# Kernel optimization log

Hardware: AMD Instinct MI355X
Metric: run time of the kernel (lower is better)

Reference implementation:

```python
import jax, jax.numpy as jnp
from jax import lax
import numpy as np

INPUT_SIZE = 1
HIDDEN = 32
NUM_LAYERS = 2
OUTPUT_SIZE = 1
FC1 = 16
B, T = 4096, 512


def _lstm_layer(x, w_ih, w_hh, b_ih, b_hh):
    """One LSTM layer, batch_first x: [B,T,in] -> outputs [B,T,H], (h_T, c_T).
    PyTorch gate order: i, f, g, o."""
    Bsz = x.shape[0]
    H = w_hh.shape[1]
    # Precompute input projections for all timesteps: [B,T,4H]
    xp = jnp.einsum('bti,gi->btg', x, w_ih) + b_ih + b_hh
    xp_t = jnp.swapaxes(xp, 0, 1)  # [T,B,4H]

    def step(carry, xt):
        h, c = carry
        gates = xt + h @ w_hh.T  # [B,4H]
        i, f, g, o = jnp.split(gates, 4, axis=-1)
        i = jax.nn.sigmoid(i)
        f = jax.nn.sigmoid(f)
        g = jnp.tanh(g)
        o = jax.nn.sigmoid(o)
        c = f * c + i * g
        h = o * jnp.tanh(c)
        return (h, c), h

    h0 = jnp.zeros((Bsz, H), dtype=x.dtype)
    c0 = jnp.zeros((Bsz, H), dtype=x.dtype)
    (hT, cT), hs = lax.scan(step, (h0, c0), xp_t)
    return jnp.swapaxes(hs, 0, 1), (hT, cT)


def setup_inputs() -> dict:
    key = jax.random.key(0)
    ks = jax.random.split(key, 12)
    s = 1.0 / np.sqrt(HIDDEN)

    def u(k, shape):
        return jax.random.uniform(k, shape, jnp.float32, -s, s)

    x = jax.random.normal(ks[0], (B, T, INPUT_SIZE), jnp.float32)
    return {
        'x': x,
        'w_ih0': u(ks[1], (4 * HIDDEN, INPUT_SIZE)),
        'w_hh0': u(ks[2], (4 * HIDDEN, HIDDEN)),
        'b_ih0': u(ks[3], (4 * HIDDEN,)),
        'b_hh0': u(ks[4], (4 * HIDDEN,)),
        'w_ih1': u(ks[5], (4 * HIDDEN, HIDDEN)),
        'w_hh1': u(ks[6], (4 * HIDDEN, HIDDEN)),
        'b_ih1': u(ks[7], (4 * HIDDEN,)),
        'b_hh1': u(ks[8], (4 * HIDDEN,)),
        'fc1_w': u(ks[9], (FC1, HIDDEN)),
        'fc1_b': jnp.zeros((FC1,), jnp.float32),
        'fc2_w': u(ks[10], (OUTPUT_SIZE, FC1)),
        'fc2_b': jnp.zeros((OUTPUT_SIZE,), jnp.float32),
    }


def reference(x, w_ih0, w_hh0, b_ih0, b_hh0, w_ih1, w_hh1, b_ih1, b_hh1,
              fc1_w, fc1_b, fc2_w, fc2_b):
    # Layer 0: need full output sequence to feed layer 1.
    h_seq, _ = _lstm_layer(x, w_ih0, w_hh0, b_ih0, b_hh0)
    # (inter-layer dropout is identity at inference)
    # Layer 1: only final hidden state is used downstream.
    _, (hT, _) = _lstm_layer(h_seq, w_ih1, w_hh1, b_ih1, b_hh1)
    # Head (dropouts identity at inference): fc1 -> relu -> fc2
    out = jax.nn.relu(hT @ fc1_w.T + fc1_b)
    out = out @ fc2_w.T + fc2_b  # [B, output_size]
    return out
```

## Files before the change

### kernel.cpp

```cpp
#include <hip/hip_runtime.h>

#define TLEN 512
#define XSTR 516
#define HSTR 40

typedef __attribute__((ext_vector_type(8))) short bf16x8;
typedef __attribute__((ext_vector_type(4))) float f32x4;

#define LOG2E_ 1.44269504f
#define S2F_   2.88539008f

__device__ __forceinline__ float fexp2_(float x) {
#if __has_builtin(__builtin_amdgcn_exp2f)
    return __builtin_amdgcn_exp2f(x);
#else
    return __expf(x * 0.69314718056f);
#endif
}
__device__ __forceinline__ float frcp_(float x) {
#if __has_builtin(__builtin_amdgcn_rcpf)
    return __builtin_amdgcn_rcpf(x);
#else
    return 1.0f / x;
#endif
}
__device__ __forceinline__ unsigned short f2bf(float f) {
    unsigned u = __float_as_uint(f);
    u += 0x7FFFu + ((u >> 16) & 1u);
    return (unsigned short)(u >> 16);
}
__device__ __forceinline__ float bf2f(unsigned short b) {
    return __uint_as_float(((unsigned)b) << 16);
}

__device__ __forceinline__ float lstm_nl(const f32x4 a, float& cS) {
    const float i_ = frcp_(1.0f + fexp2_(a[0]));
    const float f_ = frcp_(1.0f + fexp2_(a[1]));
    const float rg = frcp_(1.0f + fexp2_(a[2]));
    const float g_ = S2F_ - 2.0f * S2F_ * rg;
    const float o_ = frcp_(1.0f + fexp2_(a[3]));
    cS = f_ * cS + i_ * g_;
    const float rc = frcp_(1.0f + fexp2_(cS));
    return o_ * (1.0f - 2.0f * rc);
}

__global__ __launch_bounds__(512, 1)
void lstm2_mfma(const float* __restrict__ x,
                const float* __restrict__ w_ih0,
                const float* __restrict__ w_hh0,
                const float* __restrict__ b_ih0,
                const float* __restrict__ b_hh0,
                const float* __restrict__ w_ih1,
                const float* __restrict__ w_hh1,
                const float* __restrict__ b_ih1,
                const float* __restrict__ b_hh1,
                const float* __restrict__ fc1_w,
                const float* __restrict__ fc1_b,
                const float* __restrict__ fc2_w,
                const float* __restrict__ fc2_b,
                float* __restrict__ out)
{
    __shared__ float x_lds[16][XSTR];
    __shared__ unsigned short h0b[2][2][16][HSTR];
    __shared__ unsigned short h1b[2][2][16][HSTR];
    __shared__ float h1f[16][36];

    const int tid  = threadIdx.x;
    const int wid  = tid >> 6;
    const int lane = tid & 63;
    const int col  = lane & 15;
    const int kq   = lane >> 4;
    const int b0   = blockIdx.x * 16;

    for (int i4 = tid; i4 < (16 * TLEN) / 4; i4 += 512) {
        const int idx = i4 * 4;
        const int row = idx >> 9, cx = idx & 511;
        float4 v = *(const float4*)(x + (long)(b0 + row) * TLEN + cx);
        *(float4*)&x_lds[row][cx] = v;
    }
    for (int i = tid; i < 2 * 2 * 16 * HSTR; i += 512) {
        ((unsigned short*)h0b)[i] = 0;
        ((unsigned short*)h1b)[i] = 0;
    }

    const int tile = wid;
    const int jj   = 4 * tile + kq;
    const int k0   = kq * 8;

    const int   arow = (col & 3) * 32 + 4 * tile + (col >> 2);
    const float sA   = ((col & 3) == 2) ? S2F_ : -LOG2E_;

    bf16x8 wL0hi, wL0lo, wIhi, wIlo, wHhi, wHlo;
    #pragma unroll
    for (int e = 0; e < 8; ++e) {
        float w;
        unsigned short hb;
        w = sA * w_hh0[arow * 32 + k0 + e]; hb = f2bf(w);
        wL0hi[e] = (short)hb; wL0lo[e] = (short)f2bf(w - bf2f(hb));
        w = sA * w_ih1[arow * 32 + k0 + e]; hb = f2bf(w);
        wIhi[e]  = (short)hb; wIlo[e]  = (short)f2bf(w - bf2f(hb));
        w = sA * w_hh1[arow * 32 + k0 + e]; hb = f2bf(w);
        wHhi[e]  = (short)hb; wHlo[e]  = (short)f2bf(w - bf2f(hb));
    }

    f32x4 biasL0, biasL1, xwv;
    #pragma unroll
    for (int r = 0; r < 4; ++r) {
        const int  row = r * 32 + 4 * tile + kq;
        const float sr = (r == 2) ? S2F_ : -LOG2E_;
        biasL0[r] = sr * (b_ih0[row] + b_hh0[row]);
        biasL1[r] = sr * (b_ih1[row] + b_hh1[row]);
        xwv[r]    = sr * w_ih0[row];
    }

    float cL0 = 0.0f, cL1 = 0.0f;
    __syncthreads();

#define PACK_H(BUF, PAR, HV, J)                                                  \
    do {                                                                         \
        const unsigned u_ = __float_as_uint(HV);                                 \
        BUF[PAR][0][col][J] = (unsigned short)(u_ >> 16);                        \
        const float lof_ = (HV) - __uint_as_float(u_ & 0xFFFF0000u);             \
        BUF[PAR][1][col][J] = (unsigned short)(__float_as_uint(lof_) >> 16);     \
    } while (0)

#define STEP_BODY(T, CUR, PRV)                                                   \
    do {                                                                         \
        const int t_ = (T);                                                      \
        const bf16x8 bhi = *(const bf16x8*)&h0b[PRV][0][col][k0];                \
        const bf16x8 blo = *(const bf16x8*)&h0b[PRV][1][col][k0];                \
        if (t_ < TLEN) {                                                         \
            const float xt = x_lds[col][t_];                                     \
            f32x4 aL0 = biasL0 + xwv * xt;                                       \
            aL0 = __builtin_amdgcn_mfma_f32_16x16x32_bf16(wL0hi, bhi, aL0, 0, 0, 0); \
            aL0 = __builtin_amdgcn_mfma_f32_16x16x32_bf16(wL0hi, blo, aL0, 0, 0, 0); \
            aL0 = __builtin_amdgcn_mfma_f32_16x16x32_bf16(wL0lo, bhi, aL0, 0, 0, 0); \
            const float hv = lstm_nl(aL0, cL0);                                  \
            PACK_H(h0b, CUR, hv, jj);                                            \
        }                                                                        \
        if (t_ >= 1) {                                                           \
            const bf16x8 chi = *(const bf16x8*)&h1b[CUR][0][col][k0];            \
            const bf16x8 clo = *(const bf16x8*)&h1b[CUR][1][col][k0];            \
            f32x4 aL1 = biasL1;                                                  \
            aL1 = __builtin_amdgcn_mfma_f32_16x16x32_bf16(wIhi, bhi, aL1, 0, 0, 0); \
            aL1 = __builtin_amdgcn_mfma_f32_16x16x32_bf16(wIhi, blo, aL1, 0, 0, 0); \
            aL1 = __builtin_amdgcn_mfma_f32_16x16x32_bf16(wIlo, bhi, aL1, 0, 0, 0); \
            aL1 = __builtin_amdgcn_mfma_f32_16x16x32_bf16(wHhi, chi, aL1, 0, 0, 0); \
            aL1 = __builtin_amdgcn_mfma_f32_16x16x32_bf16(wHhi, clo, aL1, 0, 0, 0); \
            aL1 = __builtin_amdgcn_mfma_f32_16x16x32_bf16(wHlo, chi, aL1, 0, 0, 0); \
            const float hv = lstm_nl(aL1, cL1);                                  \
            PACK_H(h1b, PRV, hv, jj);                                            \
            if (t_ == TLEN) h1f[col][jj] = hv;                                   \
        }                                                                        \
        __syncthreads();                                                         \
    } while (0)

    STEP_BODY(0, 0, 1);
    for (int tt = 1; tt < TLEN; tt += 2) {
        STEP_BODY(tt,     1, 0);
        STEP_BODY(tt + 1, 0, 1);
    }
#undef STEP_BODY
#undef PACK_H

    if (wid == 0) {
        float s = 0.0f;
        #pragma unroll
        for (int it = 0; it < 4; ++it) {
            const int r = kq * 4 + it;
            float acc = fc1_b[r];
            #pragma unroll
            for (int qq = 0; qq < 8; ++qq) {
                const float4 wv = *(const float4*)(fc1_w + r * 32 + qq * 4);
                const float4 hv = *(const float4*)&h1f[col][qq * 4];
                acc += wv.x * hv.x + wv.y * hv.y + wv.z * hv.z + wv.w * hv.w;
            }
            s += fmaxf(acc, 0.0f) * fc2_w[r];
        }
        s += __shfl_xor(s, 16);
        s += __shfl_xor(s, 32);
        if (lane < 16) out[b0 + col] = s + fc2_b[0];
    }
}

extern "C" void kernel_launch(void* const* d_in, const int* in_sizes, int n_in,
                              void* d_out, int out_size, void* d_ws, size_t ws_size,
                              hipStream_t stream) {
    const float* x     = (const float*)d_in[0];
    const float* w_ih0 = (const float*)d_in[1];
    const float* w_hh0 = (const float*)d_in[2];
    const float* b_ih0 = (const float*)d_in[3];
    const float* b_hh0 = (const float*)d_in[4];
    const float* w_ih1 = (const float*)d_in[5];
    const float* w_hh1 = (const float*)d_in[6];
    const float* b_ih1 = (const float*)d_in[7];
    const float* b_hh1 = (const float*)d_in[8];
    const float* fc1_w = (const float*)d_in[9];
    const float* fc1_b = (const float*)d_in[10];
    const float* fc2_w = (const float*)d_in[11];
    const float* fc2_b = (const float*)d_in[12];
    float* out = (float*)d_out;

    dim3 grid(4096 / 16);
    dim3 block(512);
    hipLaunchKernelGGL(lstm2_mfma, grid, block, 0, stream,
                       x, w_ih0, w_hh0, b_ih0, b_hh0,
                       w_ih1, w_hh1, b_ih1, b_hh1,
                       fc1_w, fc1_b, fc2_w, fc2_b, out);
}
```

Measured before the change: 235.5 us.

## Split LSTM layers across separate wavefronts with 1024-thread blocks

Doubles the block to 16 waves: waves 0-7 compute layer 0 and waves 8-15 compute layer 1, where before each wave did both layers serially in every step. The layer-1 waves split their MFMA chain into two independent accumulators (input and recurrent) and sum them, shortening the dependency chain. The aim is a shorter per-step critical path, at the cost of twice as many waves taking part in each __syncthreads barrier and possibly more register pressure per CU.

```diff
diff --git a/kernel.cpp b/kernel.cpp
--- a/kernel.cpp
+++ b/kernel.cpp
@@ -44,7 +44,7 @@
     return o_ * (1.0f - 2.0f * rc);
 }
 
-__global__ __launch_bounds__(512, 1)
+__global__ __launch_bounds__(1024, 1)
 void lstm2_mfma(const float* __restrict__ x,
                 const float* __restrict__ w_ih0,
                 const float* __restrict__ w_hh0,
@@ -72,48 +72,50 @@
     const int kq   = lane >> 4;
     const int b0   = blockIdx.x * 16;
 
-    for (int i4 = tid; i4 < (16 * TLEN) / 4; i4 += 512) {
+    for (int i4 = tid; i4 < (16 * TLEN) / 4; i4 += 1024) {
         const int idx = i4 * 4;
         const int row = idx >> 9, cx = idx & 511;
         float4 v = *(const float4*)(x + (long)(b0 + row) * TLEN + cx);
         *(float4*)&x_lds[row][cx] = v;
     }
-    for (int i = tid; i < 2 * 2 * 16 * HSTR; i += 512) {
+    for (int i = tid; i < 2 * 2 * 16 * HSTR; i += 1024) {
         ((unsigned short*)h0b)[i] = 0;
         ((unsigned short*)h1b)[i] = 0;
     }
 
-    const int tile = wid;
-    const int jj   = 4 * tile + kq;
-    const int k0   = kq * 8;
+    const bool L0w  = (wid < 8);
+    const int  tile = wid & 7;
+    const int  jj   = 4 * tile + kq;
+    const int  k0   = kq * 8;
 
     const int   arow = (col & 3) * 32 + 4 * tile + (col >> 2);
     const float sA   = ((col & 3) == 2) ? S2F_ : -LOG2E_;
 
-    bf16x8 wL0hi, wL0lo, wIhi, wIlo, wHhi, wHlo;
-    #pragma unroll
-    for (int e = 0; e < 8; ++e) {
-        float w;
-        unsigned short hb;
-        w = sA * w_hh0[arow * 32 + k0 + e]; hb = f2bf(w);
-        wL0hi[e] = (short)hb; wL0lo[e] = (short)f2bf(w - bf2f(hb));
-        w = sA * w_ih1[arow * 32 + k0 + e]; hb = f2bf(w);
-        wIhi[e]  = (short)hb; wIlo[e]  = (short)f2bf(w - bf2f(hb));
-        w = sA * w_hh1[arow * 32 + k0 + e]; hb = f2bf(w);
-        wHhi[e]  = (short)hb; wHlo[e]  = (short)f2bf(w - bf2f(hb));
-    }
-
-    f32x4 biasL0, biasL1, xwv;
+    bf16x8 wAhi, wAlo, wHhi, wHlo;
+    {
+        const float* WA = L0w ? w_hh0 : w_ih1;
+        #pragma unroll
+        for (int e = 0; e < 8; ++e) {
+            float w;
+            unsigned short hb;
+            w = sA * WA[arow * 32 + k0 + e]; hb = f2bf(w);
+            wAhi[e] = (short)hb; wAlo[e] = (short)f2bf(w - bf2f(hb));
+            w = L0w ? 0.0f : sA * w_hh1[arow * 32 + k0 + e]; hb = f2bf(w);
+            wHhi[e] = (short)hb; wHlo[e] = (short)f2bf(w - bf2f(hb));
+        }
+    }
+
+    f32x4 biasv, xwv;
     #pragma unroll
     for (int r = 0; r < 4; ++r) {
         const int  row = r * 32 + 4 * tile + kq;
         const float sr = (r == 2) ? S2F_ : -LOG2E_;
-        biasL0[r] = sr * (b_ih0[row] + b_hh0[row]);
-        biasL1[r] = sr * (b_ih1[row] + b_hh1[row]);
-        xwv[r]    = sr * w_ih0[row];
-    }
-
-    float cL0 = 0.0f, cL1 = 0.0f;
+        biasv[r] = L0w ? sr * (b_ih0[row] + b_hh0[row])
+                       : sr * (b_ih1[row] + b_hh1[row]);
+        xwv[r]   = L0w ? sr * w_ih0[row] : 0.0f;
+    }
+
+    float cS = 0.0f;
     __syncthreads();
 
 #define PACK_H(BUF, PAR, HV, J)                                                  \
@@ -127,30 +129,37 @@
 #define STEP_BODY(T, CUR, PRV)                                                   \
     do {                                                                         \
         const int t_ = (T);                                                      \
-        const bf16x8 bhi = *(const bf16x8*)&h0b[PRV][0][col][k0];                \
-        const bf16x8 blo = *(const bf16x8*)&h0b[PRV][1][col][k0];                \
-        if (t_ < TLEN) {                                                         \
-            const float xt = x_lds[col][t_];                                     \
-            f32x4 aL0 = biasL0 + xwv * xt;                                       \
-            aL0 = __builtin_amdgcn_mfma_f32_16x16x32_bf16(wL0hi, bhi, aL0, 0, 0, 0); \
-            aL0 = __builtin_amdgcn_mfma_f32_16x16x32_bf16(wL0hi, blo, aL0, 0, 0, 0); \
-            aL0 = __builtin_amdgcn_mfma_f32_16x16x32_bf16(wL0lo, bhi, aL0, 0, 0, 0); \
-            const float hv = lstm_nl(aL0, cL0);                                  \
-            PACK_H(h0b, CUR, hv, jj);                                            \
-        }                                                                        \
-        if (t_ >= 1) {                                                           \
-            const bf16x8 chi = *(const bf16x8*)&h1b[CUR][0][col][k0];            \
-            const bf16x8 clo = *(const bf16x8*)&h1b[CUR][1][col][k0];            \
-            f32x4 aL1 = biasL1;                                                  \
-            aL1 = __builtin_amdgcn_mfma_f32_16x16x32_bf16(wIhi, bhi, aL1, 0, 0, 0); \
-            aL1 = __builtin_amdgcn_mfma_f32_16x16x32_bf16(wIhi, blo, aL1, 0, 0, 0); \
-            aL1 = __builtin_amdgcn_mfma_f32_16x16x32_bf16(wIlo, bhi, aL1, 0, 0, 0); \
-            aL1 = __builtin_amdgcn_mfma_f32_16x16x32_bf16(wHhi, chi, aL1, 0, 0, 0); \
-            aL1 = __builtin_amdgcn_mfma_f32_16x16x32_bf16(wHhi, clo, aL1, 0, 0, 0); \
-            aL1 = __builtin_amdgcn_mfma_f32_16x16x32_bf16(wHlo, chi, aL1, 0, 0, 0); \
-            const float hv = lstm_nl(aL1, cL1);                                  \
-            PACK_H(h1b, PRV, hv, jj);                                            \
-            if (t_ == TLEN) h1f[col][jj] = hv;                                   \
+        if (L0w) {                                                               \
+            if (t_ < TLEN) {                                                     \
+                const bf16x8 bhi = *(const bf16x8*)&h0b[PRV][0][col][k0];        \
+                const bf16x8 blo = *(const bf16x8*)&h0b[PRV][1][col][k0];        \
+                const float xt = x_lds[col][t_];                                 \
+                f32x4 a = biasv + xwv * xt;                                      \
+                a = __builtin_amdgcn_mfma_f32_16x16x32_bf16(wAhi, bhi, a, 0, 0, 0); \
+                a = __builtin_amdgcn_mfma_f32_16x16x32_bf16(wAhi, blo, a, 0, 0, 0); \
+                a = __builtin_amdgcn_mfma_f32_16x16x32_bf16(wAlo, bhi, a, 0, 0, 0); \
+                const float hv = lstm_nl(a, cS);                                 \
+                PACK_H(h0b, CUR, hv, jj);                                        \
+            }                                                                    \
+        } else {                                                                 \
+            if (t_ >= 1) {                                                       \
+                const bf16x8 bhi = *(const bf16x8*)&h0b[PRV][0][col][k0];        \
+                const bf16x8 blo = *(const bf16x8*)&h0b[PRV][1][col][k0];        \
+                const bf16x8 chi = *(const bf16x8*)&h1b[CUR][0][col][k0];        \
+                const bf16x8 clo = *(const bf16x8*)&h1b[CUR][1][col][k0];        \
+                f32x4 aI = biasv;                                                \
+                f32x4 aH = {0.0f, 0.0f, 0.0f, 0.0f};                             \
+                aI = __builtin_amdgcn_mfma_f32_16x16x32_bf16(wAhi, bhi, aI, 0, 0, 0); \
+                aH = __builtin_amdgcn_mfma_f32_16x16x32_bf16(wHhi, chi, aH, 0, 0, 0); \
+                aI = __builtin_amdgcn_mfma_f32_16x16x32_bf16(wAhi, blo, aI, 0, 0, 0); \
+                aH = __builtin_amdgcn_mfma_f32_16x16x32_bf16(wHhi, clo, aH, 0, 0, 0); \
+                aI = __builtin_amdgcn_mfma_f32_16x16x32_bf16(wAlo, bhi, aI, 0, 0, 0); \
+                aH = __builtin_amdgcn_mfma_f32_16x16x32_bf16(wHlo, chi, aH, 0, 0, 0); \
+                const f32x4 a = aI + aH;                                         \
+                const float hv = lstm_nl(a, cS);                                 \
+                PACK_H(h1b, PRV, hv, jj);                                        \
+                if (t_ == TLEN) h1f[col][jj] = hv;                               \
+            }                                                                    \
         }                                                                        \
         __syncthreads();                                                         \
     } while (0)
@@ -202,7 +211,7 @@
     float* out = (float*)d_out;
 
     dim3 grid(4096 / 16);
-    dim3 block(512);
+    dim3 block(1024);
     hipLaunchKernelGGL(lstm2_mfma, grid, block, 0, stream,
                        x, w_ih0, w_hh0, b_ih0, b_hh0,
                        w_ih1, w_hh1, b_ih1, b_hh1,
```

Result: slower. 264.4 us (+12.3%).

## Peel LSTM prologue/epilogue and interleave three independent MFMA accumulation chains

Applied to the files above, without the earlier changes.

Peels the first and last timesteps out of the wavefront loop so the steady-state body has no branches. The layer-1 gate sum is split into two independent accumulators (input and recurrent part), and the MFMAs of layer 0, layer-1 input and layer-1 recurrent are interleaved so their dependency chains overlap instead of running as one serial chain of six. The nonlinearities for both layers are computed together to expose more instruction-level parallelism in the exp/rcp sequence. It costs one extra vector add per step and more live registers.

```diff
diff --git a/kernel.cpp b/kernel.cpp
--- a/kernel.cpp
+++ b/kernel.cpp
@@ -33,15 +33,25 @@
     return __uint_as_float(((unsigned)b) << 16);
 }
 
-__device__ __forceinline__ float lstm_nl(const f32x4 a, float& cS) {
-    const float i_ = frcp_(1.0f + fexp2_(a[0]));
-    const float f_ = frcp_(1.0f + fexp2_(a[1]));
-    const float rg = frcp_(1.0f + fexp2_(a[2]));
-    const float g_ = S2F_ - 2.0f * S2F_ * rg;
-    const float o_ = frcp_(1.0f + fexp2_(a[3]));
-    cS = f_ * cS + i_ * g_;
-    const float rc = frcp_(1.0f + fexp2_(cS));
-    return o_ * (1.0f - 2.0f * rc);
+__device__ __forceinline__ void lstm_nl2(const f32x4 a0, const f32x4 a1,
+                                         float& c0, float& c1,
+                                         float& hv0, float& hv1) {
+    const float e00 = fexp2_(a0[0]), e01 = fexp2_(a0[1]);
+    const float e02 = fexp2_(a0[2]), e03 = fexp2_(a0[3]);
+    const float e10 = fexp2_(a1[0]), e11 = fexp2_(a1[1]);
+    const float e12 = fexp2_(a1[2]), e13 = fexp2_(a1[3]);
+    const float i0 = frcp_(1.0f + e00), f0 = frcp_(1.0f + e01);
+    const float r0 = frcp_(1.0f + e02), o0 = frcp_(1.0f + e03);
+    const float i1 = frcp_(1.0f + e10), f1 = frcp_(1.0f + e11);
+    const float r1 = frcp_(1.0f + e12), o1 = frcp_(1.0f + e13);
+    const float g0 = S2F_ - 2.0f * S2F_ * r0;
+    const float g1 = S2F_ - 2.0f * S2F_ * r1;
+    c0 = f0 * c0 + i0 * g0;
+    c1 = f1 * c1 + i1 * g1;
+    const float ec0 = fexp2_(c0), ec1 = fexp2_(c1);
+    const float rc0 = frcp_(1.0f + ec0), rc1 = frcp_(1.0f + ec1);
+    hv0 = o0 * (1.0f - 2.0f * rc0);
+    hv1 = o1 * (1.0f - 2.0f * rc1);
 }
 
 __global__ __launch_bounds__(512, 1)
@@ -124,43 +134,86 @@
         BUF[PAR][1][col][J] = (unsigned short)(__float_as_uint(lof_) >> 16);     \
     } while (0)
 
+    {
+        const bf16x8 bhi = *(const bf16x8*)&h0b[1][0][col][k0];
+        const bf16x8 blo = *(const bf16x8*)&h0b[1][1][col][k0];
+        const float xt = x_lds[col][0];
+        f32x4 aL0 = biasL0 + xwv * xt;
+        aL0 = __builtin_amdgcn_mfma_f32_16x16x32_bf16(wL0hi, bhi, aL0, 0, 0, 0);
+        aL0 = __builtin_amdgcn_mfma_f32_16x16x32_bf16(wL0hi, blo, aL0, 0, 0, 0);
+        aL0 = __builtin_amdgcn_mfma_f32_16x16x32_bf16(wL0lo, bhi, aL0, 0, 0, 0);
+        const float e0 = fexp2_(aL0[0]), e1 = fexp2_(aL0[1]);
+        const float e2 = fexp2_(aL0[2]), e3 = fexp2_(aL0[3]);
+        const float i_ = frcp_(1.0f + e0), f_ = frcp_(1.0f + e1);
+        const float r_ = frcp_(1.0f + e2), o_ = frcp_(1.0f + e3);
+        const float g_ = S2F_ - 2.0f * S2F_ * r_;
+        cL0 = f_ * cL0 + i_ * g_;
+        const float ec = fexp2_(cL0);
+        const float hv = o_ * (1.0f - 2.0f * frcp_(1.0f + ec));
+        PACK_H(h0b, 0, hv, jj);
+        __syncthreads();
+    }
+
 #define STEP_BODY(T, CUR, PRV)                                                   \
     do {                                                                         \
         const int t_ = (T);                                                      \
         const bf16x8 bhi = *(const bf16x8*)&h0b[PRV][0][col][k0];                \
         const bf16x8 blo = *(const bf16x8*)&h0b[PRV][1][col][k0];                \
-        if (t_ < TLEN) {                                                         \
-            const float xt = x_lds[col][t_];                                     \
-            f32x4 aL0 = biasL0 + xwv * xt;                                       \
-            aL0 = __builtin_amdgcn_mfma_f32_16x16x32_bf16(wL0hi, bhi, aL0, 0, 0, 0); \
-            aL0 = __builtin_amdgcn_mfma_f32_16x16x32_bf16(wL0hi, blo, aL0, 0, 0, 0); \
-            aL0 = __builtin_amdgcn_mfma_f32_16x16x32_bf16(wL0lo, bhi, aL0, 0, 0, 0); \
-            const float hv = lstm_nl(aL0, cL0);                                  \
-            PACK_H(h0b, CUR, hv, jj);                                            \
-        }                                                                        \
-        if (t_ >= 1) {                                                           \
-            const bf16x8 chi = *(const bf16x8*)&h1b[CUR][0][col][k0];            \
-            const bf16x8 clo = *(const bf16x8*)&h1b[CUR][1][col][k0];            \
-            f32x4 aL1 = biasL1;                                                  \
-            aL1 = __builtin_amdgcn_mfma_f32_16x16x32_bf16(wIhi, bhi, aL1, 0, 0, 0); \
-            aL1 = __builtin_amdgcn_mfma_f32_16x16x32_bf16(wIhi, blo, aL1, 0, 0, 0); \
-            aL1 = __builtin_amdgcn_mfma_f32_16x16x32_bf16(wIlo, bhi, aL1, 0, 0, 0); \
-            aL1 = __builtin_amdgcn_mfma_f32_16x16x32_bf16(wHhi, chi, aL1, 0, 0, 0); \
-            aL1 = __builtin_amdgcn_mfma_f32_16x16x32_bf16(wHhi, clo, aL1, 0, 0, 0); \
-            aL1 = __builtin_amdgcn_mfma_f32_16x16x32_bf16(wHlo, chi, aL1, 0, 0, 0); \
-            const float hv = lstm_nl(aL1, cL1);                                  \
-            PACK_H(h1b, PRV, hv, jj);                                            \
-            if (t_ == TLEN) h1f[col][jj] = hv;                                   \
-        }                                                                        \
+        const bf16x8 chi = *(const bf16x8*)&h1b[CUR][0][col][k0];                \
+        const bf16x8 clo = *(const bf16x8*)&h1b[CUR][1][col][k0];                \
+        const float xt = x_lds[col][t_];                                         \
+        f32x4 aL0 = biasL0 + xwv * xt;                                           \
+        f32x4 aI  = biasL1;                                                      \
+        f32x4 aH  = {0.0f, 0.0f, 0.0f, 0.0f};                                    \
+        aL0 = __builtin_amdgcn_mfma_f32_16x16x32_bf16(wL0hi, bhi, aL0, 0, 0, 0); \
+        aI  = __builtin_amdgcn_mfma_f32_16x16x32_bf16(wIhi,  bhi, aI,  0, 0, 0); \
+        aH  = __builtin_amdgcn_mfma_f32_16x16x32_bf16(wHhi,  chi, aH,  0, 0, 0); \
+        aL0 = __builtin_amdgcn_mfma_f32_16x16x32_bf16(wL0hi, blo, aL0, 0, 0, 0); \
+        aI  = __builtin_amdgcn_mfma_f32_16x16x32_bf16(wIhi,  blo, aI,  0, 0, 0); \
+        aH  = __builtin_amdgcn_mfma_f32_16x16x32_bf16(wHhi,  clo, aH,  0, 0, 0); \
+        aL0 = __builtin_amdgcn_mfma_f32_16x16x32_bf16(wL0lo, bhi, aL0, 0, 0, 0); \
+        aI  = __builtin_amdgcn_mfma_f32_16x16x32_bf16(wIlo,  bhi, aI,  0, 0, 0); \
+        aH  = __builtin_amdgcn_mfma_f32_16x16x32_bf16(wHlo,  chi, aH,  0, 0, 0); \
+        const f32x4 aL1 = aI + aH;                                               \
+        float hv0, hv1;                                                          \
+        lstm_nl2(aL0, aL1, cL0, cL1, hv0, hv1);                                  \
+        PACK_H(h0b, CUR, hv0, jj);                                               \
+        PACK_H(h1b, PRV, hv1, jj);                                               \
         __syncthreads();                                                         \
     } while (0)
 
-    STEP_BODY(0, 0, 1);
-    for (int tt = 1; tt < TLEN; tt += 2) {
+    for (int tt = 1; tt < TLEN - 1; tt += 2) {
         STEP_BODY(tt,     1, 0);
         STEP_BODY(tt + 1, 0, 1);
     }
+    STEP_BODY(TLEN - 1, 1, 0);
 #undef STEP_BODY
+
+    {
+        const bf16x8 bhi = *(const bf16x8*)&h0b[1][0][col][k0];
+        const bf16x8 blo = *(const bf16x8*)&h0b[1][1][col][k0];
+        const bf16x8 chi = *(const bf16x8*)&h1b[0][0][col][k0];
+        const bf16x8 clo = *(const bf16x8*)&h1b[0][1][col][k0];
+        f32x4 aI = biasL1;
+        f32x4 aH = {0.0f, 0.0f, 0.0f, 0.0f};
+        aI = __builtin_amdgcn_mfma_f32_16x16x32_bf16(wIhi, bhi, aI, 0, 0, 0);
+        aH = __builtin_amdgcn_mfma_f32_16x16x32_bf16(wHhi, chi, aH, 0, 0, 0);
+        aI = __builtin_amdgcn_mfma_f32_16x16x32_bf16(wIhi, blo, aI, 0, 0, 0);
+        aH = __builtin_amdgcn_mfma_f32_16x16x32_bf16(wHhi, clo, aH, 0, 0, 0);
+        aI = __builtin_amdgcn_mfma_f32_16x16x32_bf16(wIlo, bhi, aI, 0, 0, 0);
+        aH = __builtin_amdgcn_mfma_f32_16x16x32_bf16(wHlo, chi, aH, 0, 0, 0);
+        const f32x4 a = aI + aH;
+        const float e0 = fexp2_(a[0]), e1 = fexp2_(a[1]);
+        const float e2 = fexp2_(a[2]), e3 = fexp2_(a[3]);
+        const float i_ = frcp_(1.0f + e0), f_ = frcp_(1.0f + e1);
+        const float r_ = frcp_(1.0f + e2), o_ = frcp_(1.0f + e3);
+        const float g_ = S2F_ - 2.0f * S2F_ * r_;
+        cL1 = f_ * cL1 + i_ * g_;
+        const float ec = fexp2_(cL1);
+        const float hv = o_ * (1.0f - 2.0f * frcp_(1.0f + ec));
+        h1f[col][jj] = hv;
+        __syncthreads();
+    }
 #undef PACK_H
 
     if (wid == 0) {
```

After: 259.4 us. 10.2% more time.

## Split MFMA dependency chains and peel first/last LSTM steps from loop

Applied to the files above, without the earlier changes.

Peels the t=0 and t=TLEN steps out of the recurrent loop so the steady-state body has no branches. The serial MFMA accumulation chains are split into independent accumulators (two for layer 0, three for layer 1) that are summed afterwards, and the layer-0 and layer-1 MFMAs are interleaved. The x value for the next step is prefetched one step early. This shortens the critical MFMA latency chain per timestep, at the cost of extra registers and a slightly different floating-point summation order.

```diff
diff --git a/kernel.cpp b/kernel.cpp
--- a/kernel.cpp
+++ b/kernel.cpp
@@ -34,14 +34,16 @@
 }
 
 __device__ __forceinline__ float lstm_nl(const f32x4 a, float& cS) {
-    const float i_ = frcp_(1.0f + fexp2_(a[0]));
-    const float f_ = frcp_(1.0f + fexp2_(a[1]));
-    const float rg = frcp_(1.0f + fexp2_(a[2]));
-    const float g_ = S2F_ - 2.0f * S2F_ * rg;
-    const float o_ = frcp_(1.0f + fexp2_(a[3]));
+    const float e0 = fexp2_(a[0]), e1 = fexp2_(a[1]);
+    const float e2 = fexp2_(a[2]), e3 = fexp2_(a[3]);
+    const float i_ = frcp_(1.0f + e0);
+    const float f_ = frcp_(1.0f + e1);
+    const float r_ = frcp_(1.0f + e2);
+    const float o_ = frcp_(1.0f + e3);
+    const float g_ = S2F_ - 2.0f * S2F_ * r_;
     cS = f_ * cS + i_ * g_;
-    const float rc = frcp_(1.0f + fexp2_(cS));
-    return o_ * (1.0f - 2.0f * rc);
+    const float ec = fexp2_(cS);
+    return o_ * (1.0f - 2.0f * frcp_(1.0f + ec));
 }
 
 __global__ __launch_bounds__(512, 1)
@@ -112,6 +114,7 @@
         biasL1[r] = sr * (b_ih1[row] + b_hh1[row]);
         xwv[r]    = sr * w_ih0[row];
     }
+    const f32x4 zero4 = {0.0f, 0.0f, 0.0f, 0.0f};
 
     float cL0 = 0.0f, cL1 = 0.0f;
     __syncthreads();
@@ -124,43 +127,71 @@
         BUF[PAR][1][col][J] = (unsigned short)(__float_as_uint(lof_) >> 16);     \
     } while (0)
 
+    float xcur;
+    {
+        const float xt = x_lds[col][0];
+        f32x4 aL0 = biasL0 + xwv * xt;
+        const float hv = lstm_nl(aL0, cL0);
+        PACK_H(h0b, 0, hv, jj);
+        xcur = x_lds[col][1];
+        __syncthreads();
+    }
+
 #define STEP_BODY(T, CUR, PRV)                                                   \
     do {                                                                         \
         const int t_ = (T);                                                      \
         const bf16x8 bhi = *(const bf16x8*)&h0b[PRV][0][col][k0];                \
         const bf16x8 blo = *(const bf16x8*)&h0b[PRV][1][col][k0];                \
-        if (t_ < TLEN) {                                                         \
-            const float xt = x_lds[col][t_];                                     \
-            f32x4 aL0 = biasL0 + xwv * xt;                                       \
-            aL0 = __builtin_amdgcn_mfma_f32_16x16x32_bf16(wL0hi, bhi, aL0, 0, 0, 0); \
-            aL0 = __builtin_amdgcn_mfma_f32_16x16x32_bf16(wL0hi, blo, aL0, 0, 0, 0); \
-            aL0 = __builtin_amdgcn_mfma_f32_16x16x32_bf16(wL0lo, bhi, aL0, 0, 0, 0); \
-            const float hv = lstm_nl(aL0, cL0);                                  \
-            PACK_H(h0b, CUR, hv, jj);                                            \
-        }                                                                        \
-        if (t_ >= 1) {                                                           \
-            const bf16x8 chi = *(const bf16x8*)&h1b[CUR][0][col][k0];            \
-            const bf16x8 clo = *(const bf16x8*)&h1b[CUR][1][col][k0];            \
-            f32x4 aL1 = biasL1;                                                  \
-            aL1 = __builtin_amdgcn_mfma_f32_16x16x32_bf16(wIhi, bhi, aL1, 0, 0, 0); \
-            aL1 = __builtin_amdgcn_mfma_f32_16x16x32_bf16(wIhi, blo, aL1, 0, 0, 0); \
-            aL1 = __builtin_amdgcn_mfma_f32_16x16x32_bf16(wIlo, bhi, aL1, 0, 0, 0); \
-            aL1 = __builtin_amdgcn_mfma_f32_16x16x32_bf16(wHhi, chi, aL1, 0, 0, 0); \
-            aL1 = __builtin_amdgcn_mfma_f32_16x16x32_bf16(wHhi, clo, aL1, 0, 0, 0); \
-            aL1 = __builtin_amdgcn_mfma_f32_16x16x32_bf16(wHlo, chi, aL1, 0, 0, 0); \
-            const float hv = lstm_nl(aL1, cL1);                                  \
-            PACK_H(h1b, PRV, hv, jj);                                            \
-            if (t_ == TLEN) h1f[col][jj] = hv;                                   \
-        }                                                                        \
+        const bf16x8 chi = *(const bf16x8*)&h1b[CUR][0][col][k0];                \
+        const bf16x8 clo = *(const bf16x8*)&h1b[CUR][1][col][k0];                \
+        const float xnext = x_lds[col][t_ + 1];                                  \
+                       \
+        f32x4 a = __builtin_amdgcn_mfma_f32_16x16x32_bf16(wL0hi, bhi, biasL0, 0, 0, 0); \
+        f32x4 bpt = __builtin_amdgcn_mfma_f32_16x16x32_bf16(wL0hi, blo, zero4, 0, 0, 0); \
+        a = __builtin_amdgcn_mfma_f32_16x16x32_bf16(wL0lo, bhi, a, 0, 0, 0);     \
+                                            \
+        f32x4 cch = __builtin_amdgcn_mfma_f32_16x16x32_bf16(wIhi, bhi, biasL1, 0, 0, 0); \
+        f32x4 dch = __builtin_amdgcn_mfma_f32_16x16x32_bf16(wHhi, chi, zero4, 0, 0, 0); \
+        f32x4 ech = __builtin_amdgcn_mfma_f32_16x16x32_bf16(wIhi, blo, zero4, 0, 0, 0); \
+        cch = __builtin_amdgcn_mfma_f32_16x16x32_bf16(wIlo, bhi, cch, 0, 0, 0);  \
+        dch = __builtin_amdgcn_mfma_f32_16x16x32_bf16(wHlo, chi, dch, 0, 0, 0);  \
+        ech = __builtin_amdgcn_mfma_f32_16x16x32_bf16(wHhi, clo, ech, 0, 0, 0);  \
+                      \
+        f32x4 aL0 = a + bpt;                                                     \
+        aL0 += xwv * xcur;                                                       \
+        const float hv0 = lstm_nl(aL0, cL0);                                     \
+        PACK_H(h0b, CUR, hv0, jj);                                               \
+                                                    \
+        const f32x4 aL1 = (cch + dch) + ech;                                     \
+        const float hv1 = lstm_nl(aL1, cL1);                                     \
+        PACK_H(h1b, PRV, hv1, jj);                                               \
+        xcur = xnext;                                                            \
         __syncthreads();                                                         \
     } while (0)
 
-    STEP_BODY(0, 0, 1);
-    for (int tt = 1; tt < TLEN; tt += 2) {
+    for (int tt = 1; tt < TLEN - 1; tt += 2) {
         STEP_BODY(tt,     1, 0);
         STEP_BODY(tt + 1, 0, 1);
     }
+    STEP_BODY(TLEN - 1, 1, 0);
 #undef STEP_BODY
+
+    {
+        const bf16x8 bhi = *(const bf16x8*)&h0b[1][0][col][k0];
+        const bf16x8 blo = *(const bf16x8*)&h0b[1][1][col][k0];
+        const bf16x8 chi = *(const bf16x8*)&h1b[0][0][col][k0];
+        const bf16x8 clo = *(const bf16x8*)&h1b[0][1][col][k0];
+        f32x4 cch = __builtin_amdgcn_mfma_f32_16x16x32_bf16(wIhi, bhi, biasL1, 0, 0, 0);
+        f32x4 dch = __builtin_amdgcn_mfma_f32_16x16x32_bf16(wHhi, chi, zero4, 0, 0, 0);
+        f32x4 ech = __builtin_amdgcn_mfma_f32_16x16x32_bf16(wIhi, blo, zero4, 0, 0, 0);
+        cch = __builtin_amdgcn_mfma_f32_16x16x32_bf16(wIlo, bhi, cch, 0, 0, 0);
+        dch = __builtin_amdgcn_mfma_f32_16x16x32_bf16(wHlo, chi, dch, 0, 0, 0);
+        ech = __builtin_amdgcn_mfma_f32_16x16x32_bf16(wHhi, clo, ech, 0, 0, 0);
+        const f32x4 aL1 = (cch + dch) + ech;
+        const float hv = lstm_nl(aL1, cL1);
+        h1f[col][jj] = hv;
+        __syncthreads();
+    }
 #undef PACK_H
 
     if (wid == 0) {
```

Result: slower. 257.4 us (+9.3%).
